# Kernel optimization log

Hardware: AMD Instinct MI355X
Metric: run time of the kernel (lower is better)

Reference implementation:

```python
import jax, jax.numpy as jnp
import numpy as np

NH = 8          # n_heads
EPS = 1e-12     # layer_norm_eps


def _ln(x, g, b, eps=EPS):
    m = x.mean(-1, keepdims=True)
    v = jnp.var(x, axis=-1, keepdims=True)
    return (x - m) / jnp.sqrt(v + eps) * g + b


def _heads(x):
    # [B,S,H] -> [B,NH,S,H/NH]
    B, S, H = x.shape
    return x.reshape(B, S, NH, H // NH).transpose(0, 2, 1, 3)


def setup_inputs() -> dict:
    B, S, H, INNER = 32, 512, 512, 2048
    n_items = 50000
    std = 0.02
    ks = list(jax.random.split(jax.random.key(0), 20))
    inp = {}
    inp['x'] = jax.random.normal(ks[0], (B, S, H), jnp.float32)
    inp['value_input'] = jax.random.normal(ks[1], (B, S, H), jnp.float32)
    inp['beha_emb'] = jax.random.normal(ks[2], (B, S, H), jnp.float32)
    inp['pos_table'] = std * jax.random.normal(ks[3], (S, H), jnp.float32)
    names = ['q', 'k', 'v', 'pk', 'pq', 'bk', 'bq', 'd']
    for i, n in enumerate(names):
        inp['W' + n] = std * jax.random.normal(ks[4 + i], (H, H), jnp.float32)
        inp['b' + n] = jnp.zeros((H,), jnp.float32)
    inp['ln_g'] = jnp.ones((H,), jnp.float32)
    inp['ln_b'] = jnp.zeros((H,), jnp.float32)
    inp['W1'] = std * jax.random.normal(ks[12], (H, INNER), jnp.float32)
    inp['b1'] = jnp.zeros((INNER,), jnp.float32)
    inp['W2'] = std * jax.random.normal(ks[13], (INNER, H), jnp.float32)
    inp['b2'] = jnp.zeros((H,), jnp.float32)
    inp['ln2_g'] = jnp.ones((H,), jnp.float32)
    inp['ln2_b'] = jnp.zeros((H,), jnp.float32)
    inp['item_seq'] = jax.random.randint(ks[14], (B, S), 0, n_items, jnp.int32)
    return inp


def reference(x, value_input, beha_emb, pos_table, Wq, bq, Wk, bk, Wv, bv,
              Wpk, bpk, Wpq, bpq, Wbk, bbk, Wbq, bbq, Wd, bd, ln_g, ln_b,
              W1, b1, W2, b2, ln2_g, ln2_b, item_seq):
    B, S, H = x.shape
    dh = H // NH
    pos = pos_table[:S][None]  # [1,S,H] position_embedding(arange(S))

    q = _heads(x @ Wq + bq)
    k = _heads(x @ Wk + bk)
    v = _heads(value_input @ Wv + bv + value_input)  # value(value_input) + value_input
    pk = _heads(jnp.broadcast_to(pos @ Wpk + bpk, (B, S, H)))
    pq = _heads(jnp.broadcast_to(pos @ Wpq + bpq, (B, S, H)))
    bhk = _heads(beha_emb @ Wbk + bbk)
    bhq = _heads(beha_emb @ Wbq + bbq)

    # disentangled score: q.k^T + q.((beha_k+pos_k)/2)^T + ((beha_q+pos_q)/2).k^T
    scores = (jnp.einsum('bhqd,bhkd->bhqk', q, k)
              + jnp.einsum('bhqd,bhkd->bhqk', q, (bhk + pk) * 0.5)
              + jnp.einsum('bhqd,bhkd->bhqk', (bhq + pq) * 0.5, k))
    scores = scores / (dh ** 0.5)

    # causal + padding mask: (1 - mask) * -10000
    valid = item_seq > 0                              # [B,S]
    causal = jnp.tril(jnp.ones((S, S), bool))         # [S,S]
    ok = valid[:, None, None, :] & causal[None, None]
    scores = scores + jnp.where(ok, 0.0, -10000.0)

    probs = jax.nn.softmax(scores, axis=-1)
    ctx = jnp.einsum('bhqk,bhkd->bhqd', probs, v)
    ctx = ctx.transpose(0, 2, 1, 3).reshape(B, S, H)

    attn_out = _ln(ctx @ Wd + bd + x, ln_g, ln_b)

    # FeedForward (RecBole): dense1 -> gelu -> dense2 -> LN(residual)
    h = jax.nn.gelu(attn_out @ W1 + b1, approximate=False)
    h = h @ W2 + b2
    return _ln(h + attn_out, ln2_g, ln2_b)
```

## Files before the change

### kernel.cpp

```cpp
#include <hip/hip_runtime.h>
#include <math.h>


typedef unsigned short u16;
typedef __attribute__((ext_vector_type(8))) short bf16x8;
typedef __attribute__((ext_vector_type(4))) float f32x4;

#define NM 16384

__device__ __forceinline__ u16 f2b(float f) {
  union { float f; unsigned u; } x; x.f = f;
  return (u16)((x.u + 0x7fffu + ((x.u >> 16) & 1u)) >> 16);
}
__device__ __forceinline__ float b2f(u16 u) {
  union { unsigned u; float f; } x; x.u = ((unsigned)u) << 16; return x.f;
}
__device__ __forceinline__ f32x4 mfma16(bf16x8 a, bf16x8 b, f32x4 c) {
  return __builtin_amdgcn_mfma_f32_16x16x32_bf16(a, b, c, 0, 0, 0);
}
__device__ __forceinline__ void gl16(const u16* g, u16* l) {
  __builtin_amdgcn_global_load_lds(
      (const __attribute__((address_space(1))) unsigned int*)(const void*)g,
      (__attribute__((address_space(3))) unsigned int*)(void*)l, 16, 0, 0);
}
__device__ __forceinline__ bf16x8 baddv(bf16x8 a, bf16x8 b) {
  bf16x8 r;
  #pragma unroll
  for (int e = 0; e < 8; ++e) r[e] = (short)f2b(b2f((u16)a[e]) + b2f((u16)b[e]));
  return r;
}

__device__ __forceinline__ void kloop(
    const u16* __restrict__ A, const u16* __restrict__ W,
    int m0, int n0, int K, int kiters, u16* As, u16* Bs, bool vres,
    f32x4 (&acc)[4][4])
{
  const int tid = threadIdx.x;
  const int wave = tid>>6, lane = tid&63, quad = lane>>4, l16 = lane&15;
  const int wm = wave>>1, wn = wave&1;
  const int r1 = tid>>2, ch1 = (tid&3)*8;
  const u16* pA = A + (size_t)(m0+r1)*K + ch1;
  const u16* pB = W + (size_t)(n0+r1)*K + ch1;
  u16* sa = As + tid*8;  u16* sb = Bs + tid*8;
  for (int it = 0; it < kiters; ++it) {
    const int k0 = it*32;
    gl16(pA + k0, sa); gl16(pA + (size_t)64*K + k0, sa + 2048);
    gl16(pB + k0, sb); gl16(pB + (size_t)64*K + k0, sb + 2048);
    __syncthreads();
    bf16x8 af[4], bf[4];
    #pragma unroll
    for (int i = 0; i < 4; ++i)
      af[i] = *(const bf16x8*)&As[(wm*64 + i*16 + l16)*32 + quad*8];
    #pragma unroll
    for (int j = 0; j < 4; ++j)
      bf[j] = *(const bf16x8*)&Bs[(wn*64 + j*16 + l16)*32 + quad*8];
    if (vres) {
      #pragma unroll
      for (int j = 0; j < 4; ++j) {
        const int start = n0 + wn*64 + j*16;
        if ((start & ~31) == k0) {
          const int c = (start & 31) + l16;
          #pragma unroll
          for (int i = 0; i < 4; ++i)
            #pragma unroll
            for (int rr = 0; rr < 4; ++rr)
              acc[i][j][rr] += b2f(As[(wm*64 + i*16 + quad*4 + rr)*32 + c]);
        }
      }
    }
    #pragma unroll
    for (int i = 0; i < 4; ++i)
      #pragma unroll
      for (int j = 0; j < 4; ++j)
        acc[i][j] = mfma16(af[i], bf[j], acc[i][j]);
    __syncthreads();
  }
}

__device__ __forceinline__ void epi_std(
    f32x4 (&acc)[4][4], const float* __restrict__ bias,
    const u16* __restrict__ ex, int exmode, float scale, int gelu,
    u16* __restrict__ out, int m0, int n0, int N, u16* til)
{
  const int tid = threadIdx.x;
  const int wave = tid>>6, lane = tid&63, quad = lane>>4, l16 = lane&15;
  const int wm = wave>>1, wn = wave&1;
  #pragma unroll
  for (int pass = 0; pass < 2; ++pass) {
    if (wm == pass) {
      #pragma unroll
      for (int j = 0; j < 4; ++j) {
        const int c = wn*64 + j*16 + l16;
        const float bv = bias[n0 + c];
        #pragma unroll
        for (int i = 0; i < 4; ++i)
          #pragma unroll
          for (int rr = 0; rr < 4; ++rr) {
            float v = acc[i][j][rr] + bv;
            if (gelu) v = 0.5f*v*(1.0f + erff(v*0.70710678118654752f));
            til[(i*16 + quad*4 + rr)*136 + c] = f2b(v);
          }
      }
    }
    __syncthreads();
    const int r = tid>>2, ck = tid&3;
    const int gr = m0 + pass*64 + r;
    #pragma unroll
    for (int kk = 0; kk < 4; ++kk) {
      const int cc = ck*32 + kk*8, gc = n0 + cc;
      u16 e8[8];
      *(uint4*)e8 = *(const uint4*)&til[r*136 + cc];
      if (exmode) {
        const u16* ep = (exmode == 1) ? &ex[(size_t)(gr & 511)*512 + gc]
                                      : &ex[(size_t)gr*512 + gc];
        #pragma unroll
        for (int e = 0; e < 8; ++e) e8[e] = f2b((b2f(e8[e]) + b2f(ep[e]))*scale);
      } else if (scale != 1.0f) {
        #pragma unroll
        for (int e = 0; e < 8; ++e) e8[e] = f2b(b2f(e8[e])*scale);
      }
      *(uint4*)&out[(size_t)gr*N + gc] = *(uint4*)e8;
    }
    __syncthreads();
  }
}

__device__ __forceinline__ void epi_vt(
    f32x4 (&acc)[4][4], const float* __restrict__ bias,
    u16* __restrict__ Vt, int m0, int n0, u16* til)
{
  const int tid = threadIdx.x;
  const int wave = tid>>6, lane = tid&63, quad = lane>>4, l16 = lane&15;
  const int wm = wave>>1, wn = wave&1;
  const int b = m0 >> 9, s0 = m0 & 511;
  #pragma unroll
  for (int pass = 0; pass < 2; ++pass) {
    if (wn == pass) {
      #pragma unroll
      for (int j = 0; j < 4; ++j) {
        const int cl = j*16 + l16;
        const float bv = bias[n0 + pass*64 + cl];
        #pragma unroll
        for (int i = 0; i < 4; ++i)
          #pragma unroll
          for (int rr = 0; rr < 4; ++rr)
            til[cl*136 + wm*64 + i*16 + quad*4 + rr] = f2b(acc[i][j][rr] + bv);
      }
    }
    __syncthreads();
    const int cl = tid>>2, ck = tid&3;
    const int gn = n0 + pass*64 + cl, h = gn>>6, d = gn&63;
    u16* orow = Vt + ((size_t)((b*8 + h)*64 + d))*512 + s0 + ck*32;
    #pragma unroll
    for (int kk = 0; kk < 4; ++kk)
      *(uint4*)&orow[kk*8] = *(const uint4*)&til[cl*136 + ck*32 + kk*8];
    __syncthreads();
  }
}

struct PJ { const u16* A; const u16* W; const float* bias; const u16* ex;
            u16* out; float scale; int exmode; int epiv; };
struct ProjArgs { PJ p[7]; };

__global__ __launch_bounds__(256, 2) void proj_kernel(ProjArgs pa, int phaseBase) {
  __shared__ __align__(16) u16 smem[8704];
  u16* As = smem;  u16* Bs = smem + 4096;
  const PJ P = pa.p[phaseBase + (blockIdx.x >> 2)];
  const int n0 = (blockIdx.x & 3)*128, m0 = blockIdx.y*128;
  f32x4 acc[4][4] = {};
  kloop(P.A, P.W, m0, n0, 512, 16, As, Bs, P.epiv != 0, acc);
  if (P.epiv) epi_vt(acc, P.bias, P.out, m0, n0, smem);
  else        epi_std(acc, P.bias, P.ex, P.exmode, P.scale, 0, P.out, m0, n0, 512, smem);
}

template<int GELU>
__global__ __launch_bounds__(256, 2) void gemm1_kernel(
    const u16* __restrict__ A, const u16* __restrict__ W,
    const float* __restrict__ bias, u16* __restrict__ out, int N, int K)
{
  __shared__ __align__(16) u16 smem[8704];
  const int m0 = blockIdx.y*128, n0 = blockIdx.x*128;
  f32x4 acc[4][4] = {};
  kloop(A, W, m0, n0, K, K>>5, smem, smem + 4096, false, acc);
  epi_std(acc, bias, nullptr, 0, 1.0f, GELU, out, m0, n0, N, smem);
}

__global__ __launch_bounds__(256) void cast_all_kernel(
    const float* __restrict__ x, const float* __restrict__ v,
    const float* __restrict__ be, const float* __restrict__ pos,
    u16* __restrict__ xb, u16* __restrict__ vb, u16* __restrict__ bb,
    u16* __restrict__ posb)
{
  int z = blockIdx.y;
  const float* in = (z==0) ? x : (z==1) ? v : (z==2) ? be : pos;
  u16* out = (z==0) ? xb : (z==1) ? vb : (z==2) ? bb : posb;
  int n4 = (z < 3) ? (NM*512/4) : (512*512/4);
  int i = blockIdx.x*256 + threadIdx.x;
  if (i >= n4) return;
  float4 w = ((const float4*)in)[i];
  ((ushort4*)out)[i] = make_ushort4(f2b(w.x), f2b(w.y), f2b(w.z), f2b(w.w));
}

struct PrepArgs {
  const float* w[10];
  u16* o[10];
  const float* bbq; const float* bbk;
  float* Bq2; float* Bk2;
};
__global__ __launch_bounds__(256) void wprep_all_kernel(PrepArgs a) {
  int job = blockIdx.x;
  if (job == 1024) {
    for (int i = threadIdx.x; i < 512; i += 256) {
      a.Bq2[i] = 0.5f*a.bbq[i];
      a.Bk2[i] = 0.5f*a.bbk[i];
    }
    return;
  }
  int wsel, n0, k0, K, N;
  if (job < 512)      { wsel = job>>6; int t = job&63;  n0=(t&7)*64;  k0=(t>>3)*64; K=512;  N=512; }
  else if (job < 768) { wsel = 8;      int t = job-512; n0=(t&31)*64; k0=(t>>5)*64; K=512;  N=2048; }
  else                { wsel = 9;      int t = job-768; n0=(t&7)*64;  k0=(t>>3)*64; K=2048; N=512; }
  float sc = (wsel == 5 || wsel == 6) ? 0.5f : 1.0f;
  const float* in = a.w[wsel];
  u16* out = a.o[wsel];
  __shared__ __align__(16) u16 til[64*72];
  for (int idx = threadIdx.x; idx < 4096; idx += 256) {
    int r = idx>>6, c = idx&63;
    til[r*72+c] = f2b(in[(size_t)(k0+r)*N + n0+c] * sc);
  }
  __syncthreads();
  for (int idx = threadIdx.x; idx < 4096; idx += 256) {
    int r = idx>>6, c = idx&63;
    out[(size_t)(n0+r)*K + k0+c] = til[c*72+r];
  }
}

__global__ __launch_bounds__(512, 2) void attn_kernel(
    const u16* __restrict__ Qraw, const u16* __restrict__ Praw,
    const u16* __restrict__ Kraw, const u16* __restrict__ Mraw,
    const u16* __restrict__ Vt, const int* __restrict__ iseq,
    u16* __restrict__ ctx)
{
  const int qh = blockIdx.x, h = blockIdx.y, b = blockIdx.z;
  const int tid = threadIdx.x;
  const int wave = tid>>6, lane = tid&63, quad = lane>>4, l16 = lane&15;

  __shared__ __align__(16) u16 Ks[2][64*136];
  __shared__ __align__(16) u16 Vs[2][64*72];
  __shared__ __align__(16) u16 Ps[8][16*72];
  __shared__ float sel[512];

  const int q0 = qh*256;
  const int ntiles = 4*qh + 4;
  const u16* Kg = Kraw + (size_t)(b*512)*512 + h*64;
  const u16* Mg = Mraw + (size_t)(b*512)*512 + h*64;
  const u16* Vg = Vt + (size_t)((b*8 + h)*64)*512;

  if (tid < 512) sel[tid] = (iseq[b*512 + tid] > 0) ? 1.0f : 1e-30f;

  bf16x8 aq[2][4];
  #pragma unroll
  for (int s = 0; s < 2; ++s) {
    const size_t ro = (size_t)(b*512 + q0 + s*128 + wave*16 + l16)*512 + h*64;
    bf16x8 qf0 = *(const bf16x8*)&Qraw[ro + quad*8];
    bf16x8 qf1 = *(const bf16x8*)&Qraw[ro + 32 + quad*8];
    bf16x8 pf0 = *(const bf16x8*)&Praw[ro + quad*8];
    bf16x8 pf1 = *(const bf16x8*)&Praw[ro + 32 + quad*8];
    aq[s][0] = baddv(qf0, pf0); aq[s][1] = baddv(qf1, pf1);
    aq[s][2] = qf0;             aq[s][3] = qf1;
  }

  const int sr = tid>>3, sc8 = (tid&7)*8;
  uint4 kreg = *(const uint4*)&Kg[(size_t)sr*512 + sc8];
  uint4 mreg = *(const uint4*)&Mg[(size_t)sr*512 + sc8];
  uint4 vreg = *(const uint4*)&Vg[(size_t)sr*512 + sc8];

  f32x4 Ob[2][4] = {};
  float lrow[2][4] = {};
  u16* Pw = Ps[wave];
  int buf = 0;

  for (int kt = 0; kt < ntiles; ++kt) {
    const int k0 = kt*64;
    *(uint4*)&Ks[buf][sr*136 + sc8]      = kreg;
    *(uint4*)&Ks[buf][sr*136 + 64 + sc8] = mreg;
    *(uint4*)&Vs[buf][sr*72 + sc8]       = vreg;
    __syncthreads();
    if (kt + 1 < ntiles) {
      const int kn = k0 + 64;
      kreg = *(const uint4*)&Kg[(size_t)(kn + sr)*512 + sc8];
      mreg = *(const uint4*)&Mg[(size_t)(kn + sr)*512 + sc8];
      vreg = *(const uint4*)&Vg[(size_t)sr*512 + kn + sc8];
    }
    const bool act0 = (q0 + wave*16 + 15) >= k0;
    const bool act1 = (q0 + 128 + wave*16 + 15) >= k0;
    if (act1) {
      f32x4 sc[2][4] = {};
      #pragma unroll
      for (int ks = 0; ks < 4; ++ks) {
        bf16x8 bk[4];
        #pragma unroll
        for (int j = 0; j < 4; ++j)
          bk[j] = *(const bf16x8*)&Ks[buf][(j*16 + l16)*136 + ks*32 + quad*8];
        if (act0) {
          #pragma unroll
          for (int j = 0; j < 4; ++j) sc[0][j] = mfma16(aq[0][ks], bk[j], sc[0][j]);
        }
        #pragma unroll
        for (int j = 0; j < 4; ++j) sc[1][j] = mfma16(aq[1][ks], bk[j], sc[1][j]);
      }
      #pragma unroll
      for (int s = 0; s < 2; ++s) {
        if (s == 0 && !act0) continue;
        const int rb = q0 + s*128 + wave*16 + quad*4;
        float pj[4][4];
        #pragma unroll
        for (int j = 0; j < 4; ++j) {
          int col = k0 + j*16 + l16;
          float fs = sel[col];
          #pragma unroll
          for (int r = 0; r < 4; ++r) {
            float m2 = (col <= rb + r) ? fs : 1e-30f;
            pj[j][r] = __expf(sc[s][j][r]) * m2;
          }
        }
        #pragma unroll
        for (int r = 0; r < 4; ++r)
          lrow[s][r] += pj[0][r] + pj[1][r] + pj[2][r] + pj[3][r];
        #pragma unroll
        for (int j = 0; j < 4; ++j)
          #pragma unroll
          for (int r = 0; r < 4; ++r)
            Pw[(quad*4 + r)*72 + j*16 + l16] = f2b(pj[j][r]);
        #pragma unroll
        for (int c = 0; c < 4; ++c) {
          #pragma unroll
          for (int k2 = 0; k2 < 2; ++k2) {
            bf16x8 ap = *(const bf16x8*)&Pw[l16*72 + k2*32 + quad*8];
            bf16x8 bv = *(const bf16x8*)&Vs[buf][(c*16 + l16)*72 + k2*32 + quad*8];
            Ob[s][c] = mfma16(ap, bv, Ob[s][c]);
          }
        }
      }
    }
    buf ^= 1;
  }

  #pragma unroll
  for (int s = 0; s < 2; ++s) {
    #pragma unroll
    for (int r = 0; r < 4; ++r) {
      float l = lrow[s][r];
      #pragma unroll
      for (int d2 = 1; d2 < 16; d2 <<= 1) l += __shfl_xor(l, d2, 64);
      float inv = 1.0f / l;
      int grow = b*512 + q0 + s*128 + wave*16 + quad*4 + r;
      #pragma unroll
      for (int c = 0; c < 4; ++c)
        ctx[(size_t)grow*512 + h*64 + c*16 + l16] = f2b(Ob[s][c][r]*inv);
    }
  }
}

template<int RES>
__global__ __launch_bounds__(256) void ln_kernel(
    const u16* __restrict__ a, const void* __restrict__ resv,
    const float* __restrict__ g, const float* __restrict__ be,
    float* __restrict__ of, u16* __restrict__ ob)
{
  const int wave = threadIdx.x >> 6, lane = threadIdx.x & 63;
  const int row = blockIdx.x*4 + wave;
  const ushort4* pa = (const ushort4*)(a + (size_t)row*512);
  ushort4 a0 = pa[lane], a1 = pa[lane+64];
  float v[8] = { b2f(a0.x), b2f(a0.y), b2f(a0.z), b2f(a0.w),
                 b2f(a1.x), b2f(a1.y), b2f(a1.z), b2f(a1.w) };
  if (RES == 1) {
    const ushort4* pr = (const ushort4*)((const u16*)resv + (size_t)row*512);
    ushort4 u0 = pr[lane], u1 = pr[lane+64];
    v[0]+=b2f(u0.x); v[1]+=b2f(u0.y); v[2]+=b2f(u0.z); v[3]+=b2f(u0.w);
    v[4]+=b2f(u1.x); v[5]+=b2f(u1.y); v[6]+=b2f(u1.z); v[7]+=b2f(u1.w);
  } else {
    const float4* pr = (const float4*)((const float*)resv + (size_t)row*512);
    float4 r0 = pr[lane], r1 = pr[lane+64];
    v[0]+=r0.x; v[1]+=r0.y; v[2]+=r0.z; v[3]+=r0.w;
    v[4]+=r1.x; v[5]+=r1.y; v[6]+=r1.z; v[7]+=r1.w;
  }
  float s = 0.f, q = 0.f;
  #pragma unroll
  for (int e = 0; e < 8; ++e) { s += v[e]; q += v[e]*v[e]; }
  #pragma unroll
  for (int d = 1; d < 64; d <<= 1) { s += __shfl_xor(s, d, 64); q += __shfl_xor(q, d, 64); }
  float mean = s * (1.0f/512.0f);
  float var  = q * (1.0f/512.0f) - mean*mean;
  float rstd = rsqrtf(var + 1e-12f);
  float4 g0 = ((const float4*)g)[lane],  g1 = ((const float4*)g)[lane+64];
  float4 b0 = ((const float4*)be)[lane], b1 = ((const float4*)be)[lane+64];
  float o[8];
  o[0]=(v[0]-mean)*rstd*g0.x+b0.x; o[1]=(v[1]-mean)*rstd*g0.y+b0.y;
  o[2]=(v[2]-mean)*rstd*g0.z+b0.z; o[3]=(v[3]-mean)*rstd*g0.w+b0.w;
  o[4]=(v[4]-mean)*rstd*g1.x+b1.x; o[5]=(v[5]-mean)*rstd*g1.y+b1.y;
  o[6]=(v[6]-mean)*rstd*g1.z+b1.z; o[7]=(v[7]-mean)*rstd*g1.w+b1.w;
  if (of) {
    ((float4*)(of + (size_t)row*512))[lane]    = make_float4(o[0],o[1],o[2],o[3]);
    ((float4*)(of + (size_t)row*512))[lane+64] = make_float4(o[4],o[5],o[6],o[7]);
  }
  if (ob) {
    ((ushort4*)(ob + (size_t)row*512))[lane]    = make_ushort4(f2b(o[0]),f2b(o[1]),f2b(o[2]),f2b(o[3]));
    ((ushort4*)(ob + (size_t)row*512))[lane+64] = make_ushort4(f2b(o[4]),f2b(o[5]),f2b(o[6]),f2b(o[7]));
  }
}

extern "C" void kernel_launch(void* const* d_in, const int* in_sizes, int n_in,
                              void* d_out, int out_size, void* d_ws, size_t ws_size,
                              hipStream_t stream) {
  (void)in_sizes; (void)n_in; (void)out_size; (void)ws_size;
  const float* x    = (const float*)d_in[0];
  const float* vin  = (const float*)d_in[1];
  const float* beh  = (const float*)d_in[2];
  const float* pos  = (const float*)d_in[3];
  const float* bq   = (const float*)d_in[5];
  const float* bk   = (const float*)d_in[7];
  const float* bv   = (const float*)d_in[9];
  const float* bpk  = (const float*)d_in[11];
  const float* bpq  = (const float*)d_in[13];
  const float* bbk  = (const float*)d_in[15];
  const float* bbq  = (const float*)d_in[17];
  const float* bd   = (const float*)d_in[19];
  const float* ln_g = (const float*)d_in[20];
  const float* ln_b = (const float*)d_in[21];
  const float* b1   = (const float*)d_in[23];
  const float* b2   = (const float*)d_in[25];
  const float* ln2_g= (const float*)d_in[26];
  const float* ln2_b= (const float*)d_in[27];
  const int*   iseq = (const int*)d_in[28];
  float* out = (float*)d_out;
  char* ws = (char*)d_ws;

  size_t off = 0;
  auto nxt = [&](size_t sz) { size_t r = off; off += (sz + 255) & ~(size_t)255; return r; };
  size_t oWT[8]; for (int i = 0; i < 8; ++i) oWT[i] = nxt(512*512*2);
  size_t oW1T = nxt((size_t)512*2048*2);
  size_t oW2T = nxt((size_t)512*2048*2);
  size_t oBq2 = nxt(512*4);
  size_t oBk2 = nxt(512*4);
  size_t oPb  = nxt(512*512*2);
  size_t oPQ  = nxt(512*512*2);
  size_t oPK  = nxt(512*512*2);
  size_t oXb  = nxt((size_t)NM*512*2);
  size_t oVb  = nxt((size_t)NM*512*2);
  size_t oBb  = nxt((size_t)NM*512*2);
  size_t oQr  = nxt((size_t)NM*512*2);
  size_t oPr  = nxt((size_t)NM*512*2);
  size_t oKr  = nxt((size_t)NM*512*2);
  size_t oMr  = nxt((size_t)NM*512*2);
  size_t oVt  = nxt((size_t)NM*512*2);

  u16* WT[8]; for (int i = 0; i < 8; ++i) WT[i] = (u16*)(ws + oWT[i]);
  u16*   W1T  = (u16*)(ws + oW1T);
  u16*   W2T  = (u16*)(ws + oW2T);
  float* Bq2  = (float*)(ws + oBq2);
  float* Bk2  = (float*)(ws + oBk2);
  u16*   posb = (u16*)(ws + oPb);
  u16*   PQs  = (u16*)(ws + oPQ);
  u16*   PKs  = (u16*)(ws + oPK);
  u16*   xb   = (u16*)(ws + oXb);
  u16*   vb   = (u16*)(ws + oVb);
  u16*   bb   = (u16*)(ws + oBb);
  u16*   Qraw = (u16*)(ws + oQr);
  u16*   Praw = (u16*)(ws + oPr);
  u16*   Kraw = (u16*)(ws + oKr);
  u16*   Mraw = (u16*)(ws + oMr);
  u16*   Vtb  = (u16*)(ws + oVt);
  u16*   Cb   = (u16*)(ws + oVb);
  u16*   db   = (u16*)(ws + oPr);
  u16*   ab   = (u16*)(ws + oXb);
  u16*   h1b  = (u16*)(ws + oQr);
  u16*   f2   = (u16*)(ws + oVt);

  cast_all_kernel<<<dim3(8192, 4), 256, 0, stream>>>(x, vin, beh, pos, xb, vb, bb, posb);
  PrepArgs pr;
  const int wi[10] = {4, 6, 8, 10, 12, 14, 16, 18, 22, 24};
  for (int i = 0; i < 10; ++i) pr.w[i] = (const float*)d_in[wi[i]];
  for (int i = 0; i < 8; ++i)  pr.o[i] = WT[i];
  pr.o[8] = W1T; pr.o[9] = W2T;
  pr.bbq = bbq; pr.bbk = bbk; pr.Bq2 = Bq2; pr.Bk2 = Bk2;
  wprep_all_kernel<<<1025, 256, 0, stream>>>(pr);
  ProjArgs pj;
  pj.p[0] = { xb,   WT[0], bq,   nullptr, Qraw, 0.125f, 0, 0 };
  pj.p[1] = { xb,   WT[1], bk,   nullptr, Kraw, 1.0f,   0, 0 };
  pj.p[2] = { bb,   WT[6], Bq2,  PQs,     Praw, 0.125f, 1, 0 };
  pj.p[3] = { bb,   WT[5], Bk2,  PKs,     Mraw, 1.0f,   1, 0 };
  pj.p[4] = { vb,   WT[2], bv,   nullptr, Vtb,  1.0f,   0, 1 };
  pj.p[5] = { posb, WT[4], bpq,  nullptr, PQs,  0.5f,   0, 0 };
  pj.p[6] = { posb, WT[3], bpk,  nullptr, PKs,  0.5f,   0, 0 };
  proj_kernel<<<dim3(8, 4), 256, 0, stream>>>(pj, 5);
  proj_kernel<<<dim3(20, 128), 256, 0, stream>>>(pj, 0);
  attn_kernel<<<dim3(2, 8, 32), 512, 0, stream>>>(Qraw, Praw, Kraw, Mraw, Vtb, iseq, Cb);
  gemm1_kernel<0><<<dim3(4, 128), 256, 0, stream>>>(Cb, WT[7], bd, db, 512, 512);
  ln_kernel<0><<<4096, 256, 0, stream>>>(db, x, ln_g, ln_b, nullptr, ab);
  gemm1_kernel<1><<<dim3(16, 128), 256, 0, stream>>>(ab, W1T, b1, h1b, 2048, 512);
  gemm1_kernel<0><<<dim3(4, 128), 256, 0, stream>>>(h1b, W2T, b2, f2, 512, 2048);
  ln_kernel<1><<<4096, 256, 0, stream>>>(f2, ab, ln2_g, ln2_b, out, nullptr);
}
```

Measured before the change: 515.8 us.

## Widen GEMM tiles to 128x256 sharing A loads and balance causal attention rows

The projection and FFN GEMMs now compute two 128-column output tiles per block, sharing each staged A tile between two weight tiles. Paired projections (Q/K, beha q/k, pos q/k, V halves) run in one block, which halves A-tile global traffic and block count. The attention kernel now pairs query row blocks symmetrically (qh and 3-qh) so both blocks along x do similar causal work. The cost is more registers (two accumulator sets), more shared memory per block, and fewer blocks for the N=512 GEMMs, so occupancy and SM fill may drop.

```diff
diff --git a/kernel.cpp b/kernel.cpp
--- a/kernel.cpp
+++ b/kernel.cpp
@@ -30,49 +30,65 @@
   return r;
 }
 
-__device__ __forceinline__ void kloop(
-    const u16* __restrict__ A, const u16* __restrict__ W,
-    int m0, int n0, int K, int kiters, u16* As, u16* Bs, bool vres,
-    f32x4 (&acc)[4][4])
+__device__ __forceinline__ void kloop2(
+    const u16* __restrict__ A, const u16* __restrict__ W1,
+    const u16* __restrict__ W2, int m0, int n0a, int n0b, int K, int kiters,
+    u16* As, u16* B1, u16* B2, bool vres,
+    f32x4 (&acc1)[4][4], f32x4 (&acc2)[4][4])
 {
   const int tid = threadIdx.x;
   const int wave = tid>>6, lane = tid&63, quad = lane>>4, l16 = lane&15;
   const int wm = wave>>1, wn = wave&1;
   const int r1 = tid>>2, ch1 = (tid&3)*8;
-  const u16* pA = A + (size_t)(m0+r1)*K + ch1;
-  const u16* pB = W + (size_t)(n0+r1)*K + ch1;
-  u16* sa = As + tid*8;  u16* sb = Bs + tid*8;
+  const u16* pA  = A  + (size_t)(m0 +r1)*K + ch1;
+  const u16* pB1 = W1 + (size_t)(n0a+r1)*K + ch1;
+  const u16* pB2 = W2 + (size_t)(n0b+r1)*K + ch1;
+  u16* sa = As + tid*8;  u16* s1 = B1 + tid*8;  u16* s2 = B2 + tid*8;
   for (int it = 0; it < kiters; ++it) {
     const int k0 = it*32;
-    gl16(pA + k0, sa); gl16(pA + (size_t)64*K + k0, sa + 2048);
-    gl16(pB + k0, sb); gl16(pB + (size_t)64*K + k0, sb + 2048);
-    __syncthreads();
-    bf16x8 af[4], bf[4];
+    gl16(pA  + k0, sa); gl16(pA  + (size_t)64*K + k0, sa + 2048);
+    gl16(pB1 + k0, s1); gl16(pB1 + (size_t)64*K + k0, s1 + 2048);
+    gl16(pB2 + k0, s2); gl16(pB2 + (size_t)64*K + k0, s2 + 2048);
+    __syncthreads();
+    bf16x8 af[4], bf[4], bg[4];
     #pragma unroll
     for (int i = 0; i < 4; ++i)
       af[i] = *(const bf16x8*)&As[(wm*64 + i*16 + l16)*32 + quad*8];
     #pragma unroll
-    for (int j = 0; j < 4; ++j)
-      bf[j] = *(const bf16x8*)&Bs[(wn*64 + j*16 + l16)*32 + quad*8];
+    for (int j = 0; j < 4; ++j) {
+      bf[j] = *(const bf16x8*)&B1[(wn*64 + j*16 + l16)*32 + quad*8];
+      bg[j] = *(const bf16x8*)&B2[(wn*64 + j*16 + l16)*32 + quad*8];
+    }
     if (vres) {
       #pragma unroll
       for (int j = 0; j < 4; ++j) {
-        const int start = n0 + wn*64 + j*16;
-        if ((start & ~31) == k0) {
-          const int c = (start & 31) + l16;
+        const int s1c = n0a + wn*64 + j*16;
+        if ((s1c & ~31) == k0) {
+          const int c = (s1c & 31) + l16;
           #pragma unroll
           for (int i = 0; i < 4; ++i)
             #pragma unroll
             for (int rr = 0; rr < 4; ++rr)
-              acc[i][j][rr] += b2f(As[(wm*64 + i*16 + quad*4 + rr)*32 + c]);
+              acc1[i][j][rr] += b2f(As[(wm*64 + i*16 + quad*4 + rr)*32 + c]);
+        }
+        const int s2c = n0b + wn*64 + j*16;
+        if ((s2c & ~31) == k0) {
+          const int c = (s2c & 31) + l16;
+          #pragma unroll
+          for (int i = 0; i < 4; ++i)
+            #pragma unroll
+            for (int rr = 0; rr < 4; ++rr)
+              acc2[i][j][rr] += b2f(As[(wm*64 + i*16 + quad*4 + rr)*32 + c]);
         }
       }
     }
     #pragma unroll
     for (int i = 0; i < 4; ++i)
       #pragma unroll
-      for (int j = 0; j < 4; ++j)
-        acc[i][j] = mfma16(af[i], bf[j], acc[i][j]);
+      for (int j = 0; j < 4; ++j) {
+        acc1[i][j] = mfma16(af[i], bf[j], acc1[i][j]);
+        acc2[i][j] = mfma16(af[i], bg[j], acc2[i][j]);
+      }
     __syncthreads();
   }
 }
@@ -111,8 +127,7 @@
       u16 e8[8];
       *(uint4*)e8 = *(const uint4*)&til[r*136 + cc];
       if (exmode) {
-        const u16* ep = (exmode == 1) ? &ex[(size_t)(gr & 511)*512 + gc]
-                                      : &ex[(size_t)gr*512 + gc];
+        const u16* ep = &ex[(size_t)(gr & 511)*512 + gc];
         #pragma unroll
         for (int e = 0; e < 8; ++e) e8[e] = f2b((b2f(e8[e]) + b2f(ep[e]))*scale);
       } else if (scale != 1.0f) {
@@ -158,31 +173,49 @@
   }
 }
 
-struct PJ { const u16* A; const u16* W; const float* bias; const u16* ex;
-            u16* out; float scale; int exmode; int epiv; };
-struct ProjArgs { PJ p[7]; };
-
-__global__ __launch_bounds__(256, 2) void proj_kernel(ProjArgs pa, int phaseBase) {
-  __shared__ __align__(16) u16 smem[8704];
-  u16* As = smem;  u16* Bs = smem + 4096;
-  const PJ P = pa.p[phaseBase + (blockIdx.x >> 2)];
-  const int n0 = (blockIdx.x & 3)*128, m0 = blockIdx.y*128;
-  f32x4 acc[4][4] = {};
-  kloop(P.A, P.W, m0, n0, 512, 16, As, Bs, P.epiv != 0, acc);
-  if (P.epiv) epi_vt(acc, P.bias, P.out, m0, n0, smem);
-  else        epi_std(acc, P.bias, P.ex, P.exmode, P.scale, 0, P.out, m0, n0, 512, smem);
+struct PJ2 { const u16* A; const u16* W1; const u16* W2;
+             const float* b1; const float* b2;
+             const u16* ex1; const u16* ex2;
+             u16* o1; u16* o2; float sc1; float sc2;
+             int ex1m; int ex2m; int dn; int epiv; };
+struct ProjArgs { PJ2 p[4]; };
+
+__global__ __launch_bounds__(256, 2) void proj_kernel(ProjArgs pa, int mode) {
+  __shared__ __align__(16) u16 smem[12288];
+  u16* As = smem;  u16* B1 = smem + 4096;  u16* B2 = smem + 8192;
+  int pi, nidx;
+  if (mode) { pi = 3; nidx = blockIdx.x; }
+  else if (blockIdx.x < 4)  { pi = 0; nidx = blockIdx.x; }
+  else if (blockIdx.x < 8)  { pi = 1; nidx = blockIdx.x - 4; }
+  else                      { pi = 2; nidx = blockIdx.x - 8; }
+  const PJ2 P = pa.p[pi];
+  const int n0a = nidx*128, n0b = n0a + P.dn;
+  const int m0 = blockIdx.y*128;
+  f32x4 acc1[4][4] = {};  f32x4 acc2[4][4] = {};
+  kloop2(P.A, P.W1, P.W2, m0, n0a, n0b, 512, 16, As, B1, B2, P.epiv != 0,
+         acc1, acc2);
+  if (P.epiv) {
+    epi_vt(acc1, P.b1, P.o1, m0, n0a, smem);
+    epi_vt(acc2, P.b2, P.o2, m0, n0b, smem);
+  } else {
+    epi_std(acc1, P.b1, P.ex1, P.ex1m, P.sc1, 0, P.o1, m0, n0a, 512, smem);
+    epi_std(acc2, P.b2, P.ex2, P.ex2m, P.sc2, 0, P.o2, m0, n0b, 512, smem);
+  }
 }
 
 template<int GELU>
-__global__ __launch_bounds__(256, 2) void gemm1_kernel(
+__global__ __launch_bounds__(256, 2) void gemm2_kernel(
     const u16* __restrict__ A, const u16* __restrict__ W,
     const float* __restrict__ bias, u16* __restrict__ out, int N, int K)
 {
-  __shared__ __align__(16) u16 smem[8704];
-  const int m0 = blockIdx.y*128, n0 = blockIdx.x*128;
-  f32x4 acc[4][4] = {};
-  kloop(A, W, m0, n0, K, K>>5, smem, smem + 4096, false, acc);
-  epi_std(acc, bias, nullptr, 0, 1.0f, GELU, out, m0, n0, N, smem);
+  __shared__ __align__(16) u16 smem[12288];
+  const int m0 = blockIdx.y*128;
+  const int n0a = blockIdx.x*256, n0b = n0a + 128;
+  f32x4 acc1[4][4] = {};  f32x4 acc2[4][4] = {};
+  kloop2(A, W, W, m0, n0a, n0b, K, K>>5, smem, smem + 4096, smem + 8192,
+         false, acc1, acc2);
+  epi_std(acc1, bias, nullptr, 0, 1.0f, GELU, out, m0, n0a, N, smem);
+  epi_std(acc2, bias, nullptr, 0, 1.0f, GELU, out, m0, n0b, N, smem);
 }
 
 __global__ __launch_bounds__(256) void cast_all_kernel(
@@ -250,8 +283,8 @@
   __shared__ __align__(16) u16 Ps[8][16*72];
   __shared__ float sel[512];
 
-  const int q0 = qh*256;
-  const int ntiles = 4*qh + 4;
+  const int sbase[2] = { qh*128, (3 - qh)*128 };
+  const int ntiles = qh ? 6 : 8;
   const u16* Kg = Kraw + (size_t)(b*512)*512 + h*64;
   const u16* Mg = Mraw + (size_t)(b*512)*512 + h*64;
   const u16* Vg = Vt + (size_t)((b*8 + h)*64)*512;
@@ -261,7 +294,7 @@
   bf16x8 aq[2][4];
   #pragma unroll
   for (int s = 0; s < 2; ++s) {
-    const size_t ro = (size_t)(b*512 + q0 + s*128 + wave*16 + l16)*512 + h*64;
+    const size_t ro = (size_t)(b*512 + sbase[s] + wave*16 + l16)*512 + h*64;
     bf16x8 qf0 = *(const bf16x8*)&Qraw[ro + quad*8];
     bf16x8 qf1 = *(const bf16x8*)&Qraw[ro + 32 + quad*8];
     bf16x8 pf0 = *(const bf16x8*)&Praw[ro + quad*8];
@@ -292,8 +325,8 @@
       mreg = *(const uint4*)&Mg[(size_t)(kn + sr)*512 + sc8];
       vreg = *(const uint4*)&Vg[(size_t)sr*512 + kn + sc8];
     }
-    const bool act0 = (q0 + wave*16 + 15) >= k0;
-    const bool act1 = (q0 + 128 + wave*16 + 15) >= k0;
+    const bool act0 = (sbase[0] + wave*16 + 15) >= k0;
+    const bool act1 = (sbase[1] + wave*16 + 15) >= k0;
     if (act1) {
       f32x4 sc[2][4] = {};
       #pragma unroll
@@ -312,7 +345,7 @@
       #pragma unroll
       for (int s = 0; s < 2; ++s) {
         if (s == 0 && !act0) continue;
-        const int rb = q0 + s*128 + wave*16 + quad*4;
+        const int rb = sbase[s] + wave*16 + quad*4;
         float pj[4][4];
         #pragma unroll
         for (int j = 0; j < 4; ++j) {
@@ -354,7 +387,7 @@
       #pragma unroll
       for (int d2 = 1; d2 < 16; d2 <<= 1) l += __shfl_xor(l, d2, 64);
       float inv = 1.0f / l;
-      int grow = b*512 + q0 + s*128 + wave*16 + quad*4 + r;
+      int grow = b*512 + sbase[s] + wave*16 + quad*4 + r;
       #pragma unroll
       for (int c = 0; c < 4; ++c)
         ctx[(size_t)grow*512 + h*64 + c*16 + l16] = f2b(Ob[s][c][r]*inv);
@@ -486,19 +519,20 @@
   pr.bbq = bbq; pr.bbk = bbk; pr.Bq2 = Bq2; pr.Bk2 = Bk2;
   wprep_all_kernel<<<1025, 256, 0, stream>>>(pr);
   ProjArgs pj;
-  pj.p[0] = { xb,   WT[0], bq,   nullptr, Qraw, 0.125f, 0, 0 };
-  pj.p[1] = { xb,   WT[1], bk,   nullptr, Kraw, 1.0f,   0, 0 };
-  pj.p[2] = { bb,   WT[6], Bq2,  PQs,     Praw, 0.125f, 1, 0 };
-  pj.p[3] = { bb,   WT[5], Bk2,  PKs,     Mraw, 1.0f,   1, 0 };
-  pj.p[4] = { vb,   WT[2], bv,   nullptr, Vtb,  1.0f,   0, 1 };
-  pj.p[5] = { posb, WT[4], bpq,  nullptr, PQs,  0.5f,   0, 0 };
-  pj.p[6] = { posb, WT[3], bpk,  nullptr, PKs,  0.5f,   0, 0 };
-  proj_kernel<<<dim3(8, 4), 256, 0, stream>>>(pj, 5);
-  proj_kernel<<<dim3(20, 128), 256, 0, stream>>>(pj, 0);
+  pj.p[0] = { xb,   WT[0], WT[1], bq,  bk,  nullptr, nullptr, Qraw, Kraw,
+              0.125f, 1.0f, 0, 0, 0,   0 };
+  pj.p[1] = { bb,   WT[6], WT[5], Bq2, Bk2, PQs,     PKs,     Praw, Mraw,
+              0.125f, 1.0f, 1, 1, 0,   0 };
+  pj.p[2] = { vb,   WT[2], WT[2], bv,  bv,  nullptr, nullptr, Vtb,  Vtb,
+              1.0f,   1.0f, 0, 0, 256, 1 };
+  pj.p[3] = { posb, WT[4], WT[3], bpq, bpk, nullptr, nullptr, PQs,  PKs,
+              0.5f,   0.5f, 0, 0, 0,   0 };
+  proj_kernel<<<dim3(4, 4), 256, 0, stream>>>(pj, 1);
+  proj_kernel<<<dim3(10, 128), 256, 0, stream>>>(pj, 0);
   attn_kernel<<<dim3(2, 8, 32), 512, 0, stream>>>(Qraw, Praw, Kraw, Mraw, Vtb, iseq, Cb);
-  gemm1_kernel<0><<<dim3(4, 128), 256, 0, stream>>>(Cb, WT[7], bd, db, 512, 512);
+  gemm2_kernel<0><<<dim3(2, 128), 256, 0, stream>>>(Cb, WT[7], bd, db, 512, 512);
   ln_kernel<0><<<4096, 256, 0, stream>>>(db, x, ln_g, ln_b, nullptr, ab);
-  gemm1_kernel<1><<<dim3(16, 128), 256, 0, stream>>>(ab, W1T, b1, h1b, 2048, 512);
-  gemm1_kernel<0><<<dim3(4, 128), 256, 0, stream>>>(h1b, W2T, b2, f2, 512, 2048);
+  gemm2_kernel<1><<<dim3(8, 128), 256, 0, stream>>>(ab, W1T, b1, h1b, 2048, 512);
+  gemm2_kernel<0><<<dim3(2, 128), 256, 0, stream>>>(h1b, W2T, b2, f2, 512, 2048);
   ln_kernel<1><<<4096, 256, 0, stream>>>(f2, ab, ln2_g, ln2_b, out, nullptr);
 }
```

Measured after the change: 595.4 us. 15.4% more time.
